# Optimization experiments

Hardware: AMD Instinct MI355X
Metric: run time of the kernel (lower is better)

The kernel has to match this reference:

```python
import jax, jax.numpy as jnp
import numpy as np

C = 256
CQK = C // 8


def setup_inputs() -> dict:
    key = jax.random.key(0)
    ks = jax.random.split(key, 8)
    B, H, W = 4, 64, 64
    inputs = jax.random.normal(ks[0], (B, H, W, C), dtype=jnp.float32)
    s = 1.0 / np.sqrt(C)
    Wq = jax.random.normal(ks[1], (C, CQK), dtype=jnp.float32) * s
    bq = jnp.zeros((CQK,), dtype=jnp.float32)
    Wk = jax.random.normal(ks[2], (C, CQK), dtype=jnp.float32) * s
    bk = jnp.zeros((CQK,), dtype=jnp.float32)
    Wv = jax.random.normal(ks[3], (C, C), dtype=jnp.float32) * s
    bv = jnp.zeros((C,), dtype=jnp.float32)
    gamma = jnp.float32(0.7)  # nonzero so attention branch contributes
    return {"inputs": inputs, "Wq": Wq, "bq": bq, "Wk": Wk, "bk": bk,
            "Wv": Wv, "bv": bv, "gamma": gamma}


def reference(inputs, Wq, bq, Wk, bk, Wv, bv, gamma):
    B, H, W, Cin = inputs.shape
    N = H * W
    x = inputs.reshape(B, N, Cin)
    # 1x1 convs == per-pixel channel matmuls
    q = x @ Wq + bq                      # (B, N, C//8)
    k = x @ Wk + bk                      # (B, N, C//8)
    v = x @ Wv + bv                      # (B, N, C)
    energy = jnp.einsum('bnd,bmd->bnm', q, k)   # (B, N, N), no scale (faithful)
    attn = jax.nn.softmax(energy, axis=-1)
    x_out = jnp.einsum('bnm,bmc->bnc', attn, v)  # (B, N, C)
    out = gamma * x_out.reshape(B, H, W, Cin) + inputs
    return out
```

## Files before the change

kernel.cpp:

```cpp
#include <hip/hip_runtime.h>
#include <hip/hip_bf16.h>

#define B_ 4
#define N_ 4096
#define C_ 256
#define D_ 32
#define LOG2E 1.44269504088896340736f
#define MFMA16 __builtin_amdgcn_mfma_f32_16x16x32_bf16

typedef __attribute__((ext_vector_type(8))) short short8;
typedef __attribute__((ext_vector_type(4))) short short4v;
typedef __attribute__((ext_vector_type(4))) float float4v;

__device__ inline short f2bf_rne(float f) {
  unsigned u = __builtin_bit_cast(unsigned, f);
  u += 0x7FFFu + ((u >> 16) & 1u);
  return (short)(u >> 16);
}
__device__ inline float bf2f(short s) {
  unsigned u = ((unsigned)(unsigned short)s) << 16;
  return __builtin_bit_cast(float, u);
}
__device__ inline float fast_exp2(float x) { return __builtin_amdgcn_exp2f(x); }

__global__ __launch_bounds__(256) void cast_w_kernel(
    const float* __restrict__ Wq, const float* __restrict__ Wk,
    const float* __restrict__ Wv, short* __restrict__ WtF) {
  int i  = blockIdx.x * 256 + threadIdx.x;
  int j  = i & 7;
  int l  = (i >> 3) & 63;
  int ks = (i >> 9) & 7;
  int nb = i >> 12;
  int n  = nb * 16 + (l & 15);
  int k  = ks * 32 + ((l >> 4) << 3) + j;
  float v;
  if (n < 32)      v = Wq[k * 32 + n] * LOG2E;
  else if (n < 64) v = Wk[k * 32 + (n - 32)];
  else             v = Wv[k * 256 + (n - 64)];
  WtF[i] = f2bf_rne(v);
}

__global__ __launch_bounds__(256, 2) void proj_kernel(
    const float* __restrict__ x, const short* __restrict__ WtF,
    const float* __restrict__ bq, const float* __restrict__ bk,
    const float* __restrict__ bv,
    short* __restrict__ qb, short* __restrict__ kF, short* __restrict__ vF) {
  int blk = blockIdx.x;
  int b  = blk >> 7;
  int r0 = (blk & 127) * 32;
  int t  = threadIdx.x;
  int w  = t >> 6;
  int l  = t & 63;
  int lc = l & 15;
  int q4 = l >> 4;

  __shared__ __align__(16) short sA[32][272];
  __shared__ __align__(16) short sV[256][40];
  __shared__ __align__(16) short sK[32][36];

  {
    const float* xb = x + (size_t)(b * N_ + r0) * C_;
#pragma unroll
    for (int ch = 0; ch < 8; ch++) {
      int f   = ch * 256 + t;
      int row = f >> 6;
      int col = (f & 63) * 4;
      float4v v = *(const float4v*)(xb + f * 4);
      short4v s;
      s[0] = f2bf_rne(v[0]); s[1] = f2bf_rne(v[1]);
      s[2] = f2bf_rne(v[2]); s[3] = f2bf_rne(v[3]);
      *(short4v*)(&sA[row][col]) = s;
    }
  }
  __syncthreads();

  float4v acc[10];
#pragma unroll
  for (int i = 0; i < 10; i++) { acc[i][0] = 0.f; acc[i][1] = 0.f; acc[i][2] = 0.f; acc[i][3] = 0.f; }

  const short* wbase = WtF + w * 4096 + l * 8;

#define LOADW(B0, B1, B2, B3, B4, KS)                       \
  B0 = *(const short8*)(wbase + (KS) * 512 + 0 * 16384);    \
  B1 = *(const short8*)(wbase + (KS) * 512 + 1 * 16384);    \
  B2 = *(const short8*)(wbase + (KS) * 512 + 2 * 16384);    \
  B3 = *(const short8*)(wbase + (KS) * 512 + 3 * 16384);    \
  B4 = *(const short8*)(wbase + (KS) * 512 + 4 * 16384);

#define DO_MFMA(A0, A1, B0, B1, B2, B3, B4)                 \
  acc[0] = MFMA16(A0, B0, acc[0], 0, 0, 0);                 \
  acc[1] = MFMA16(A1, B0, acc[1], 0, 0, 0);                 \
  acc[2] = MFMA16(A0, B1, acc[2], 0, 0, 0);                 \
  acc[3] = MFMA16(A1, B1, acc[3], 0, 0, 0);                 \
  acc[4] = MFMA16(A0, B2, acc[4], 0, 0, 0);                 \
  acc[5] = MFMA16(A1, B2, acc[5], 0, 0, 0);                 \
  acc[6] = MFMA16(A0, B3, acc[6], 0, 0, 0);                 \
  acc[7] = MFMA16(A1, B3, acc[7], 0, 0, 0);                 \
  acc[8] = MFMA16(A0, B4, acc[8], 0, 0, 0);                 \
  acc[9] = MFMA16(A1, B4, acc[9], 0, 0, 0);

  short8 wA0, wA1, wA2, wA3, wA4, wB0, wB1, wB2, wB3, wB4;
  LOADW(wA0, wA1, wA2, wA3, wA4, 0)
#pragma unroll
  for (int kk = 0; kk < 8; kk += 2) {
    short8 a00 = *(const short8*)(&sA[lc][kk * 32 + q4 * 8]);
    short8 a01 = *(const short8*)(&sA[16 + lc][kk * 32 + q4 * 8]);
    LOADW(wB0, wB1, wB2, wB3, wB4, kk + 1)
    DO_MFMA(a00, a01, wA0, wA1, wA2, wA3, wA4)
    short8 a10 = *(const short8*)(&sA[lc][(kk + 1) * 32 + q4 * 8]);
    short8 a11 = *(const short8*)(&sA[16 + lc][(kk + 1) * 32 + q4 * 8]);
    LOADW(wA0, wA1, wA2, wA3, wA4, kk + 2)
    DO_MFMA(a10, a11, wB0, wB1, wB2, wB3, wB4)
  }
#undef LOADW
#undef DO_MFMA

  {
    float bias0 = (w < 2) ? bq[w * 16 + lc] * LOG2E : bk[(w - 2) * 16 + lc];
#pragma unroll
    for (int rt = 0; rt < 2; rt++) {
      if (w < 2) {
#pragma unroll
        for (int r = 0; r < 4; r++) {
          int row = rt * 16 + q4 * 4 + r;
          qb[(size_t)(b * N_ + r0 + row) * D_ + w * 16 + lc] =
              f2bf_rne(acc[rt][r] + bias0);
        }
      } else {
#pragma unroll
        for (int r = 0; r < 4; r++) {
          int row = rt * 16 + q4 * 4 + r;
          sK[row][(w - 2) * 16 + lc] = f2bf_rne(acc[rt][r] + bias0);
        }
      }
    }
#pragma unroll
    for (int nbo = 1; nbo < 5; nbo++) {
      float bias = bv[(nbo - 1) * 64 + w * 16 + lc];
#pragma unroll
      for (int rt = 0; rt < 2; rt++) {
        float4v a = acc[nbo * 2 + rt];
        short4v pk;
        pk[0] = f2bf_rne(a[0] + bias); pk[1] = f2bf_rne(a[1] + bias);
        pk[2] = f2bf_rne(a[2] + bias); pk[3] = f2bf_rne(a[3] + bias);
        *(short4v*)(&sV[(nbo - 1) * 64 + w * 16 + lc][rt * 16 + q4 * 4]) = pk;
      }
    }
  }
  __syncthreads();

  int kt  = r0 >> 6;
  int ks0 = (r0 >> 5) & 1;

  {
    size_t tb2 = ((size_t)(b * 64 + kt) * 32 + ks0 * 16) * 512;
    int cb = t >> 4;
#pragma unroll
    for (int k = 0; k < 4; k++) {
      int p = (t & 15) * 4 + k;
      int j = p >> 4, i = p & 15;
      short8 vv = *(const short8*)(&sV[cb * 16 + i][j * 8]);
      *(short8*)(vF + tb2 + (size_t)t * 32 + k * 8) = vv;
    }
  }
  if (t < 128) {
    int fr = t >> 6, ll = t & 63;
    int kv = fr * 16 + (ll & 15), dg = ll >> 4;
    size_t tbk = ((size_t)(b * 64 + kt) * 4 + ks0 * 2) * 512;
    short8 kv8 = *(const short8*)(&sK[kv][dg * 8]);
    *(short8*)(kF + tbk + (size_t)t * 8) = kv8;
  }
}

__global__ __launch_bounds__(512, 4) void flash_partial_kernel(
    const short* __restrict__ qb, const short* __restrict__ kF,
    const short* __restrict__ vF, short* __restrict__ obuf,
    float* __restrict__ lbuf) {
  int blk = blockIdx.x;
  int b  = blk & 3;
  int hb = (blk >> 2) & 1;
  int qt = blk >> 3;
  int r0 = qt * 64;
  int t  = threadIdx.x;
  int w  = t >> 6;
  int l  = t & 63;
  int lc = l & 15;
  int q4 = l >> 4;
  int rq = w & 3;
  int cq = w & 3;
  bool qkw = (w < 4);

  __shared__ __align__(16) short sP[2][64][72];

  int p = (b * 64 + qt) * 2 + hb;

  short8 qf = *(const short8*)(qb + (size_t)(b * N_ + r0 + rq * 16 + lc) * D_ + q4 * 8);

  const short* kbp = kF + ((size_t)(b * 64 + hb * 32) * 4) * 512 + l * 8;
  const short* vbp = vF + ((size_t)(b * 64 + hb * 32) * 32 + cq * 4) * 512 + l * 8;

  short8 kC0, kC1, kC2, kC3;
  short8 vC[8];

  if (qkw) {
    kC0 = *(const short8*)(kbp + 0);
    kC1 = *(const short8*)(kbp + 512);
    kC2 = *(const short8*)(kbp + 1024);
    kC3 = *(const short8*)(kbp + 1536);
  } else {
#pragma unroll
    for (int ks = 0; ks < 2; ks++)
#pragma unroll
      for (int cb = 0; cb < 4; cb++)
        vC[ks * 4 + cb] = *(const short8*)(vbp + ks * 8192 + cb * 512);
  }

  float4v O[16];
#pragma unroll
  for (int i = 0; i < 16; i++) { O[i][0] = 0.f; O[i][1] = 0.f; O[i][2] = 0.f; O[i][3] = 0.f; }
  float l_part = 0.f;

#define K_RELOAD(TI)                                                           \
  { size_t o_ = (size_t)(TI) * 2048;                                           \
    kC0 = *(const short8*)(kbp + o_);                                          \
    kC1 = *(const short8*)(kbp + o_ + 512);                                    \
    kC2 = *(const short8*)(kbp + o_ + 1024);                                   \
    kC3 = *(const short8*)(kbp + o_ + 1536); }

#define V_RELOAD(TI)                                                           \
  { size_t vo = (size_t)(TI) * 16384;                                          \
    _Pragma("unroll")                                                          \
    for (int ks = 0; ks < 2; ks++)                                             \
      _Pragma("unroll")                                                        \
      for (int cb = 0; cb < 4; cb++)                                           \
        vC[ks * 4 + cb] = *(const short8*)(vbp + vo + ks * 8192 + cb * 512); }

#define QK_STEP(SPB, VALID)                                                    \
  { float4v z; z[0] = 0.f; z[1] = 0.f; z[2] = 0.f; z[3] = 0.f;                 \
    float4v S0 = MFMA16(kC0, qf, z, 0, 0, 0);                                  \
    float4v S1 = MFMA16(kC1, qf, z, 0, 0, 0);                                  \
    float4v S2 = MFMA16(kC2, qf, z, 0, 0, 0);                                  \
    float4v S3 = MFMA16(kC3, qf, z, 0, 0, 0);                                  \
    short* rowp = &sP[SPB][rq * 16 + lc][q4 * 4];                              \
    float ts = 0.f;                                                            \
    { float p0 = fast_exp2(S0[0]), p1 = fast_exp2(S0[1]);                      \
      float p2 = fast_exp2(S0[2]), p3 = fast_exp2(S0[3]);                      \
      ts += (p0 + p1) + (p2 + p3);                                             \
      short4v pk; pk[0] = f2bf_rne(p0); pk[1] = f2bf_rne(p1);                  \
      pk[2] = f2bf_rne(p2); pk[3] = f2bf_rne(p3);                              \
      *(short4v*)(rowp + 0) = pk; }                                            \
    { float p0 = fast_exp2(S1[0]), p1 = fast_exp2(S1[1]);                      \
      float p2 = fast_exp2(S1[2]), p3 = fast_exp2(S1[3]);                      \
      ts += (p0 + p1) + (p2 + p3);                                             \
      short4v pk; pk[0] = f2bf_rne(p0); pk[1] = f2bf_rne(p1);                  \
      pk[2] = f2bf_rne(p2); pk[3] = f2bf_rne(p3);                              \
      *(short4v*)(rowp + 16) = pk; }                                           \
    { float p0 = fast_exp2(S2[0]), p1 = fast_exp2(S2[1]);                      \
      float p2 = fast_exp2(S2[2]), p3 = fast_exp2(S2[3]);                      \
      ts += (p0 + p1) + (p2 + p3);                                             \
      short4v pk; pk[0] = f2bf_rne(p0); pk[1] = f2bf_rne(p1);                  \
      pk[2] = f2bf_rne(p2); pk[3] = f2bf_rne(p3);                              \
      *(short4v*)(rowp + 32) = pk; }                                           \
    { float p0 = fast_exp2(S3[0]), p1 = fast_exp2(S3[1]);                      \
      float p2 = fast_exp2(S3[2]), p3 = fast_exp2(S3[3]);                      \
      ts += (p0 + p1) + (p2 + p3);                                             \
      short4v pk; pk[0] = f2bf_rne(p0); pk[1] = f2bf_rne(p1);                  \
      pk[2] = f2bf_rne(p2); pk[3] = f2bf_rne(p3);                              \
      *(short4v*)(rowp + 48) = pk; }                                           \
    if (VALID) l_part += ts; }

#define PV_STEP(SPB)                                                           \
  { _Pragma("unroll")                                                          \
    for (int rt = 0; rt < 4; rt++) {                                           \
      short8 pf0 = *(const short8*)(&sP[SPB][rt * 16 + lc][q4 * 8]);           \
      short8 pf1 = *(const short8*)(&sP[SPB][rt * 16 + lc][32 + q4 * 8]);      \
      _Pragma("unroll")                                                        \
      for (int cb = 0; cb < 4; cb++) {                                         \
        O[rt * 4 + cb] = MFMA16(pf0, vC[cb],     O[rt * 4 + cb], 0, 0, 0);     \
        O[rt * 4 + cb] = MFMA16(pf1, vC[4 + cb], O[rt * 4 + cb], 0, 0, 0);     \
      }                                                                        \
    } }

  if (qkw) {
    QK_STEP(0, true)
    K_RELOAD(1)
  }
  __syncthreads();

  for (int ti = 0; ti < 32; ti += 2) {
    int n1 = ti + 1;
    int n2 = (ti + 2 < 32) ? ti + 2 : 31;
    bool v2 = (ti + 2 < 32);
    int n3 = (ti + 3 < 32) ? ti + 3 : 31;

    if (qkw) {
      QK_STEP(1, true)
      K_RELOAD(n2)
    } else {
      PV_STEP(0)
      V_RELOAD(n1)
    }
    __syncthreads();

    if (qkw) {
      QK_STEP(0, v2)
      K_RELOAD(n3)
    } else {
      PV_STEP(1)
      V_RELOAD(n2)
    }
    __syncthreads();
  }
#undef K_RELOAD
#undef V_RELOAD
#undef QK_STEP
#undef PV_STEP

  if (!qkw) {
    short* ob = obuf + ((size_t)p * 64 + cq * 16) * 256 + l * 4;
#pragma unroll
    for (int a = 0; a < 16; a++) {
      float4v o = O[a];
      short4v pk;
      pk[0] = f2bf_rne(o[0]); pk[1] = f2bf_rne(o[1]);
      pk[2] = f2bf_rne(o[2]); pk[3] = f2bf_rne(o[3]);
      *(short4v*)(ob + a * 256) = pk;
    }
  } else {
    float l_tot = l_part + __shfl_xor(l_part, 16, 64);
    l_tot += __shfl_xor(l_tot, 32, 64);
    if (q4 == 0) lbuf[(size_t)p * 64 + rq * 16 + lc] = l_tot;
  }
}

__global__ __launch_bounds__(256) void merge_kernel(
    const short* __restrict__ obuf, const float* __restrict__ lbuf,
    const float* __restrict__ xin, const float* __restrict__ gptr,
    float* __restrict__ out) {
  int blk = blockIdx.x;
  int t   = threadIdx.x;
  float g = *gptr;

  __shared__ float sS[32][260];
  __shared__ float sLinv[64];

  const short* o0 = obuf + (size_t)(blk * 2 + 0) * 16384;
  const short* o1 = obuf + (size_t)(blk * 2 + 1) * 16384;
  const float* l0 = lbuf + (size_t)(blk * 2 + 0) * 64;
  const float* l1 = lbuf + (size_t)(blk * 2 + 1) * 64;
  size_t gbase = (size_t)blk * 16384;

  if (t < 64) sLinv[t] = __builtin_amdgcn_rcpf(l0[t] + l1[t]);

#pragma unroll
  for (int h = 0; h < 2; h++) {
#pragma unroll
    for (int j = 0; j < 4; j++) {
      int gdx  = j * 256 + t;
      int ucq  = gdx >> 8;
      int rem  = gdx & 255;
      int jj   = rem >> 5;
      int pos8 = rem & 31;
      int offs = (ucq * 16 + h * 8 + jj) * 256 + pos8 * 8;
      short8 a8 = *(const short8*)(o0 + offs);
      short8 c8 = *(const short8*)(o1 + offs);
      int rtl = jj >> 2;
      int cb  = jj & 3;
      int chB = ucq * 64 + cb * 16;
#pragma unroll
      for (int e = 0; e < 8; e++) {
        int lane = pos8 * 2 + (e >> 2);
        int r    = e & 3;
        int row  = rtl * 16 + (lane >> 4) * 4 + r;
        int ch   = chB + (lane & 15);
        sS[row][ch] = bf2f(a8[e]) + bf2f(c8[e]);
      }
    }
    __syncthreads();

#pragma unroll
    for (int j = 0; j < 8; j++) {
      int gdx = j * 1024 + t * 4;
      int row = 32 * h + (gdx >> 8);
      int ch  = gdx & 255;
      float linv = sLinv[row];
      size_t gi = gbase + (size_t)(32 * h) * 256 + gdx;
      float4v xv = *(const float4v*)(xin + gi);
      float4v sv = *(const float4v*)(&sS[row - 32 * h][ch]);
      float4v ov;
#pragma unroll
      for (int e = 0; e < 4; e++) ov[e] = g * (sv[e] * linv) + xv[e];
      *(float4v*)(out + gi) = ov;
    }
    __syncthreads();
  }
}

extern "C" void kernel_launch(void* const* d_in, const int* in_sizes, int n_in,
                              void* d_out, int out_size, void* d_ws, size_t ws_size,
                              hipStream_t stream) {
  const float* x     = (const float*)d_in[0];
  const float* Wq    = (const float*)d_in[1];
  const float* bq    = (const float*)d_in[2];
  const float* Wk    = (const float*)d_in[3];
  const float* bk    = (const float*)d_in[4];
  const float* Wv    = (const float*)d_in[5];
  const float* bv    = (const float*)d_in[6];
  const float* gamma = (const float*)d_in[7];
  float* out = (float*)d_out;

  char* ws = (char*)d_ws;
  short* qb   = (short*)ws;
  short* kF   = (short*)(ws + (1u << 20));
  short* vF   = (short*)(ws + (2u << 20));
  short* WtF  = (short*)(ws + (10u << 20));
  short* obuf = (short*)(ws + (11u << 20));
  float* lbuf = (float*)(ws + (28u << 20));

  hipLaunchKernelGGL(cast_w_kernel,        dim3(320), dim3(256), 0, stream, Wq, Wk, Wv, WtF);
  hipLaunchKernelGGL(proj_kernel,          dim3(512), dim3(256), 0, stream, x, WtF, bq, bk, bv, qb, kF, vF);
  hipLaunchKernelGGL(flash_partial_kernel, dim3(512), dim3(512), 0, stream, qb, kF, vF, obuf, lbuf);
  hipLaunchKernelGGL(merge_kernel,         dim3(256), dim3(256), 0, stream, obuf, lbuf, x, gamma, out);
}
```

Before: 156.0 us.

## Halve flash query tile to 32 rows and let all waves share PV work

The flash partial kernel now handles 32 query rows per block instead of 64, doubling the grid to 1024 blocks and raising the launch-bounds occupancy hint to 8. Instead of splitting waves into QK-only and PV-only groups, all 8 waves now do PV on a 32-channel slice while 2 waves also compute QK/softmax. The merge kernel is resized to match. This aims to improve occupancy and balance wave work, but each block re-reads K/V for fewer queries, which doubles K/V global traffic and adds per-tile syncs.

```diff
diff --git a/kernel.cpp b/kernel.cpp
--- a/kernel.cpp
+++ b/kernel.cpp
@@ -172,7 +172,7 @@
   }
 }
 
-__global__ __launch_bounds__(512, 4) void flash_partial_kernel(
+__global__ __launch_bounds__(512, 8) void flash_partial_kernel(
     const short* __restrict__ qb, const short* __restrict__ kF,
     const short* __restrict__ vF, short* __restrict__ obuf,
     float* __restrict__ lbuf) {
@@ -180,44 +180,41 @@
   int b  = blk & 3;
   int hb = (blk >> 2) & 1;
   int qt = blk >> 3;
-  int r0 = qt * 64;
+  int r0 = qt * 32;
   int t  = threadIdx.x;
   int w  = t >> 6;
   int l  = t & 63;
   int lc = l & 15;
   int q4 = l >> 4;
-  int rq = w & 3;
-  int cq = w & 3;
-  bool qkw = (w < 4);
-
-  __shared__ __align__(16) short sP[2][64][72];
-
-  int p = (b * 64 + qt) * 2 + hb;
+  int rq = w & 1;
+  bool qkw = (w < 2);
+
+  __shared__ __align__(16) short sP[2][32][72];
+
+  int p = (b * 128 + qt) * 2 + hb;
 
   short8 qf = *(const short8*)(qb + (size_t)(b * N_ + r0 + rq * 16 + lc) * D_ + q4 * 8);
 
   const short* kbp = kF + ((size_t)(b * 64 + hb * 32) * 4) * 512 + l * 8;
-  const short* vbp = vF + ((size_t)(b * 64 + hb * 32) * 32 + cq * 4) * 512 + l * 8;
+  const short* vbp = vF + ((size_t)(b * 64 + hb * 32) * 32 + 2 * w) * 512 + l * 8;
 
   short8 kC0, kC1, kC2, kC3;
-  short8 vC[8];
+  short8 vC0, vC1, vC2, vC3;
 
   if (qkw) {
     kC0 = *(const short8*)(kbp + 0);
     kC1 = *(const short8*)(kbp + 512);
     kC2 = *(const short8*)(kbp + 1024);
     kC3 = *(const short8*)(kbp + 1536);
-  } else {
-#pragma unroll
-    for (int ks = 0; ks < 2; ks++)
-#pragma unroll
-      for (int cb = 0; cb < 4; cb++)
-        vC[ks * 4 + cb] = *(const short8*)(vbp + ks * 8192 + cb * 512);
-  }
-
-  float4v O[16];
-#pragma unroll
-  for (int i = 0; i < 16; i++) { O[i][0] = 0.f; O[i][1] = 0.f; O[i][2] = 0.f; O[i][3] = 0.f; }
+  }
+  vC0 = *(const short8*)(vbp + 0);
+  vC1 = *(const short8*)(vbp + 512);
+  vC2 = *(const short8*)(vbp + 8192);
+  vC3 = *(const short8*)(vbp + 8704);
+
+  float4v O[4];
+#pragma unroll
+  for (int i = 0; i < 4; i++) { O[i][0] = 0.f; O[i][1] = 0.f; O[i][2] = 0.f; O[i][3] = 0.f; }
   float l_part = 0.f;
 
 #define K_RELOAD(TI)                                                           \
@@ -229,11 +226,10 @@
 
 #define V_RELOAD(TI)                                                           \
   { size_t vo = (size_t)(TI) * 16384;                                          \
-    _Pragma("unroll")                                                          \
-    for (int ks = 0; ks < 2; ks++)                                             \
-      _Pragma("unroll")                                                        \
-      for (int cb = 0; cb < 4; cb++)                                           \
-        vC[ks * 4 + cb] = *(const short8*)(vbp + vo + ks * 8192 + cb * 512); }
+    vC0 = *(const short8*)(vbp + vo);                                          \
+    vC1 = *(const short8*)(vbp + vo + 512);                                    \
+    vC2 = *(const short8*)(vbp + vo + 8192);                                   \
+    vC3 = *(const short8*)(vbp + vo + 8704); }
 
 #define QK_STEP(SPB, VALID)                                                    \
   { float4v z; z[0] = 0.f; z[1] = 0.f; z[2] = 0.f; z[3] = 0.f;                 \
@@ -271,14 +267,13 @@
 
 #define PV_STEP(SPB)                                                           \
   { _Pragma("unroll")                                                          \
-    for (int rt = 0; rt < 4; rt++) {                                           \
-      short8 pf0 = *(const short8*)(&sP[SPB][rt * 16 + lc][q4 * 8]);           \
-      short8 pf1 = *(const short8*)(&sP[SPB][rt * 16 + lc][32 + q4 * 8]);      \
-      _Pragma("unroll")                                                        \
-      for (int cb = 0; cb < 4; cb++) {                                         \
-        O[rt * 4 + cb] = MFMA16(pf0, vC[cb],     O[rt * 4 + cb], 0, 0, 0);     \
-        O[rt * 4 + cb] = MFMA16(pf1, vC[4 + cb], O[rt * 4 + cb], 0, 0, 0);     \
-      }                                                                        \
+    for (int rt2 = 0; rt2 < 2; rt2++) {                                        \
+      short8 pf0 = *(const short8*)(&sP[SPB][rt2 * 16 + lc][q4 * 8]);          \
+      short8 pf1 = *(const short8*)(&sP[SPB][rt2 * 16 + lc][32 + q4 * 8]);     \
+      O[rt2 * 2 + 0] = MFMA16(pf0, vC0, O[rt2 * 2 + 0], 0, 0, 0);              \
+      O[rt2 * 2 + 0] = MFMA16(pf1, vC2, O[rt2 * 2 + 0], 0, 0, 0);              \
+      O[rt2 * 2 + 1] = MFMA16(pf0, vC1, O[rt2 * 2 + 1], 0, 0, 0);              \
+      O[rt2 * 2 + 1] = MFMA16(pf1, vC3, O[rt2 * 2 + 1], 0, 0, 0);              \
     } }
 
   if (qkw) {
@@ -296,19 +291,17 @@
     if (qkw) {
       QK_STEP(1, true)
       K_RELOAD(n2)
-    } else {
-      PV_STEP(0)
-      V_RELOAD(n1)
-    }
+    }
+    PV_STEP(0)
+    V_RELOAD(n1)
     __syncthreads();
 
     if (qkw) {
       QK_STEP(0, v2)
       K_RELOAD(n3)
-    } else {
-      PV_STEP(1)
-      V_RELOAD(n2)
-    }
+    }
+    PV_STEP(1)
+    V_RELOAD(n2)
     __syncthreads();
   }
 #undef K_RELOAD
@@ -316,20 +309,21 @@
 #undef QK_STEP
 #undef PV_STEP
 
-  if (!qkw) {
-    short* ob = obuf + ((size_t)p * 64 + cq * 16) * 256 + l * 4;
-#pragma unroll
-    for (int a = 0; a < 16; a++) {
+  {
+    short* ob = obuf + ((size_t)p * 32 + w * 4) * 256 + l * 4;
+#pragma unroll
+    for (int a = 0; a < 4; a++) {
       float4v o = O[a];
       short4v pk;
       pk[0] = f2bf_rne(o[0]); pk[1] = f2bf_rne(o[1]);
       pk[2] = f2bf_rne(o[2]); pk[3] = f2bf_rne(o[3]);
       *(short4v*)(ob + a * 256) = pk;
     }
-  } else {
+  }
+  if (qkw) {
     float l_tot = l_part + __shfl_xor(l_part, 16, 64);
     l_tot += __shfl_xor(l_tot, 32, 64);
-    if (q4 == 0) lbuf[(size_t)p * 64 + rq * 16 + lc] = l_tot;
+    if (q4 == 0) lbuf[(size_t)p * 32 + rq * 16 + lc] = l_tot;
   }
 }
 
@@ -342,57 +336,53 @@
   float g = *gptr;
 
   __shared__ float sS[32][260];
-  __shared__ float sLinv[64];
-
-  const short* o0 = obuf + (size_t)(blk * 2 + 0) * 16384;
-  const short* o1 = obuf + (size_t)(blk * 2 + 1) * 16384;
-  const float* l0 = lbuf + (size_t)(blk * 2 + 0) * 64;
-  const float* l1 = lbuf + (size_t)(blk * 2 + 1) * 64;
-  size_t gbase = (size_t)blk * 16384;
-
-  if (t < 64) sLinv[t] = __builtin_amdgcn_rcpf(l0[t] + l1[t]);
-
-#pragma unroll
-  for (int h = 0; h < 2; h++) {
-#pragma unroll
-    for (int j = 0; j < 4; j++) {
-      int gdx  = j * 256 + t;
-      int ucq  = gdx >> 8;
-      int rem  = gdx & 255;
-      int jj   = rem >> 5;
-      int pos8 = rem & 31;
-      int offs = (ucq * 16 + h * 8 + jj) * 256 + pos8 * 8;
-      short8 a8 = *(const short8*)(o0 + offs);
-      short8 c8 = *(const short8*)(o1 + offs);
-      int rtl = jj >> 2;
-      int cb  = jj & 3;
-      int chB = ucq * 64 + cb * 16;
-#pragma unroll
-      for (int e = 0; e < 8; e++) {
-        int lane = pos8 * 2 + (e >> 2);
-        int r    = e & 3;
-        int row  = rtl * 16 + (lane >> 4) * 4 + r;
-        int ch   = chB + (lane & 15);
-        sS[row][ch] = bf2f(a8[e]) + bf2f(c8[e]);
-      }
-    }
-    __syncthreads();
-
-#pragma unroll
-    for (int j = 0; j < 8; j++) {
-      int gdx = j * 1024 + t * 4;
-      int row = 32 * h + (gdx >> 8);
-      int ch  = gdx & 255;
-      float linv = sLinv[row];
-      size_t gi = gbase + (size_t)(32 * h) * 256 + gdx;
-      float4v xv = *(const float4v*)(xin + gi);
-      float4v sv = *(const float4v*)(&sS[row - 32 * h][ch]);
-      float4v ov;
-#pragma unroll
-      for (int e = 0; e < 4; e++) ov[e] = g * (sv[e] * linv) + xv[e];
-      *(float4v*)(out + gi) = ov;
-    }
-    __syncthreads();
+  __shared__ float sLinv[32];
+
+  const short* o0 = obuf + (size_t)(blk * 2 + 0) * 8192;
+  const short* o1 = obuf + (size_t)(blk * 2 + 1) * 8192;
+  const float* l0 = lbuf + (size_t)(blk * 2 + 0) * 32;
+  const float* l1 = lbuf + (size_t)(blk * 2 + 1) * 32;
+  size_t gbase = (size_t)blk * 8192;
+
+  if (t < 32) sLinv[t] = __builtin_amdgcn_rcpf(l0[t] + l1[t]);
+
+#pragma unroll
+  for (int j = 0; j < 4; j++) {
+    int gdx  = j * 256 + t;
+    int w8   = gdx >> 7;
+    int within = gdx & 127;
+    int s_in = within >> 5;
+    int pos8 = within & 31;
+    int offs = (w8 * 4 + s_in) * 256 + pos8 * 8;
+    short8 a8 = *(const short8*)(o0 + offs);
+    short8 c8 = *(const short8*)(o1 + offs);
+    int rt2 = s_in >> 1;
+    int cbo = s_in & 1;
+    int chB = w8 * 32 + cbo * 16;
+#pragma unroll
+    for (int e = 0; e < 8; e++) {
+      int lane = pos8 * 2 + (e >> 2);
+      int r    = e & 3;
+      int row  = rt2 * 16 + (lane >> 4) * 4 + r;
+      int ch   = chB + (lane & 15);
+      sS[row][ch] = bf2f(a8[e]) + bf2f(c8[e]);
+    }
+  }
+  __syncthreads();
+
+#pragma unroll
+  for (int j = 0; j < 8; j++) {
+    int gdx = j * 1024 + t * 4;
+    int row = gdx >> 8;
+    int ch  = gdx & 255;
+    float linv = sLinv[row];
+    size_t gi = gbase + gdx;
+    float4v xv = *(const float4v*)(xin + gi);
+    float4v sv = *(const float4v*)(&sS[row][ch]);
+    float4v ov;
+#pragma unroll
+    for (int e = 0; e < 4; e++) ov[e] = g * (sv[e] * linv) + xv[e];
+    *(float4v*)(out + gi) = ov;
   }
 }
 
@@ -417,8 +407,8 @@
   short* obuf = (short*)(ws + (11u << 20));
   float* lbuf = (float*)(ws + (28u << 20));
 
-  hipLaunchKernelGGL(cast_w_kernel,        dim3(320), dim3(256), 0, stream, Wq, Wk, Wv, WtF);
-  hipLaunchKernelGGL(proj_kernel,          dim3(512), dim3(256), 0, stream, x, WtF, bq, bk, bv, qb, kF, vF);
-  hipLaunchKernelGGL(flash_partial_kernel, dim3(512), dim3(512), 0, stream, qb, kF, vF, obuf, lbuf);
-  hipLaunchKernelGGL(merge_kernel,         dim3(256), dim3(256), 0, stream, obuf, lbuf, x, gamma, out);
-}
+  hipLaunchKernelGGL(cast_w_kernel,        dim3(320),  dim3(256), 0, stream, Wq, Wk, Wv, WtF);
+  hipLaunchKernelGGL(proj_kernel,          dim3(512),  dim3(256), 0, stream, x, WtF, bq, bk, bv, qb, kF, vF);
+  hipLaunchKernelGGL(flash_partial_kernel, dim3(1024), dim3(512), 0, stream, qb, kF, vF, obuf, lbuf);
+  hipLaunchKernelGGL(merge_kernel,         dim3(512),  dim3(256), 0, stream, obuf, lbuf, x, gamma, out);
+}
```

Result: slower. 169.3 us (+8.5%).
